# Performance work log

Measured on AMD Instinct MI355X. Metric: run time of the kernel, lower is better.

The kernel has to match this reference:

```python
import jax, jax.numpy as jnp
import numpy as np

INV_TEMP = 100.0


def setup_inputs() -> dict:
    key = jax.random.key(0)
    k1, k2, k3 = jax.random.split(key, 3)
    B, C, J, Hh, Wh = 64, 4, 17, 96, 96
    heatmaps = jax.random.normal(k1, (B * C, J, Hh, Wh), dtype=jnp.float32)
    projection_matrices = jax.random.normal(k2, (B, C, 3, 4), dtype=jnp.float32)
    confidences = jax.random.uniform(k3, (B, C, J), dtype=jnp.float32)
    return {
        "heatmaps": heatmaps,
        "projection_matrices": projection_matrices,
        "confidences": confidences,
        "H_img": 384,
        "W_img": 384,
    }


def _softargmax(heatmaps):
    # heatmaps: (B*C, J, Hh, Wh) -> keypoints (B*C, J, 2) as (x, y)
    bc, J, Hh, Wh = heatmaps.shape
    hm = jax.nn.softmax((heatmaps * INV_TEMP).reshape(bc, J, Hh * Wh), axis=-1)
    hm = hm.reshape(bc, J, Hh, Wh)
    xs = jnp.arange(Wh, dtype=hm.dtype)
    ys = jnp.arange(Hh, dtype=hm.dtype)
    kx = jnp.einsum('bjhw,w->bj', hm, xs)  # x = width index (grid c=0)
    ky = jnp.einsum('bjhw,h->bj', hm, ys)  # y = height index (grid c=1)
    return jnp.stack([kx, ky], axis=-1)


def _dlt(P, kp2d, conf):
    # P: (B,C,3,4), kp2d: (B,C,J,2), conf: (B,C,J) -> (B,J,3)
    B, C, J = kp2d.shape[:3]
    # A[b,c,j,i,:] = P[b,c,2,:]*kp2d[b,c,j,i] - P[b,c,i,:], scaled by conf
    A = (P[:, :, None, 2:3, :] * kp2d[:, :, :, :, None]
         - P[:, :, None, :2, :]) * conf[:, :, :, None, None]  # (B,C,J,2,4)
    A = A.transpose(0, 2, 1, 3, 4).reshape(B, J, 2 * C, 4)
    _, _, Vh = jnp.linalg.svd(A, full_matrices=False)  # Vh: (B,J,4,4)
    homo = Vh[..., 3, :]  # smallest right singular vector, (B,J,4)
    return homo[..., :3] / homo[..., 3:4]


def reference(heatmaps, projection_matrices, confidences, H_img, W_img):
    B, C = projection_matrices.shape[:2]
    bc, J, Hh, Wh = heatmaps.shape
    kp = _softargmax(heatmaps)  # (B*C, J, 2)
    # faithful (quirky) rescale: x *= H/Hh, y *= W/Wh as in original code
    scale = jnp.array([H_img / Hh, W_img / Wh], dtype=kp.dtype)
    kp = (kp * scale).reshape(B, C, J, 2)
    return _dlt(projection_matrices, kp, confidences)
```

## Files before the change

kernel.cpp:

```cpp
#include <hip/hip_runtime.h>

#define B_NUM 64
#define C_NUM 4
#define J_NUM 17
#define HH 96
#define WW 96
#define HWSZ (HH * WW)

__device__ __forceinline__ float waveMax(float v) {
#pragma unroll
  for (int o = 32; o > 0; o >>= 1) v = fmaxf(v, __shfl_xor(v, o));
  return v;
}
__device__ __forceinline__ float waveSum(float v) {
#pragma unroll
  for (int o = 32; o > 0; o >>= 1) v += __shfl_xor(v, o);
  return v;
}

__global__ __launch_bounds__(256) void softargmax_k(
    const float* __restrict__ hm, const int* __restrict__ Hp,
    const int* __restrict__ Wp, float* __restrict__ kp) {
  const int r = blockIdx.x;
  const int t = threadIdx.x;
  const float4* row = (const float4*)(hm + (size_t)r * HWSZ);

  float m = -3.4e38f;
  float se = 0.f, sx = 0.f, sy = 0.f;
#pragma unroll
  for (int k = 0; k < 9; ++k) {
    const float4 v = row[k * 256 + t];
    const int base = k * 1024 + t * 4;
    const int h = base / WW;
    const int w0 = base - h * WW;
    const float c = fmaxf(fmaxf(v.x, v.y), fmaxf(v.z, v.w));
    const float mn = fmaxf(m, c);
    const float f = __expf(100.f * (m - mn));
    m = mn;
    se *= f; sx *= f; sy *= f;
    const float a = -100.f * mn;
    const float e0 = __expf(fmaf(100.f, v.x, a));
    const float e1 = __expf(fmaf(100.f, v.y, a));
    const float e2 = __expf(fmaf(100.f, v.z, a));
    const float e3 = __expf(fmaf(100.f, v.w, a));
    const float esum = (e0 + e1) + (e2 + e3);
    se += esum;
    sy = fmaf(esum, (float)h, sy);
    sx += fmaf(esum, (float)w0, fmaf(2.f, e2, fmaf(3.f, e3, e1)));
  }

  const float M = waveMax(m);
  const float fw = __expf(100.f * (m - M));
  se = waveSum(se * fw);
  sx = waveSum(sx * fw);
  sy = waveSum(sy * fw);

  __shared__ float s[4][4];
  const int wid = t >> 6, lane = t & 63;
  if (lane == 0) { s[wid][0] = M; s[wid][1] = se; s[wid][2] = sx; s[wid][3] = sy; }
  __syncthreads();
  if (t == 0) {
    const float MM = fmaxf(fmaxf(s[0][0], s[1][0]), fmaxf(s[2][0], s[3][0]));
    float SE = 0.f, SX = 0.f, SY = 0.f;
#pragma unroll
    for (int i = 0; i < 4; ++i) {
      const float f = __expf(100.f * (s[i][0] - MM));
      SE = fmaf(s[i][1], f, SE);
      SX = fmaf(s[i][2], f, SX);
      SY = fmaf(s[i][3], f, SY);
    }
    const float scx = (float)Hp[0] / (float)HH;
    const float scy = (float)Wp[0] / (float)WW;
    ((float2*)kp)[r] = make_float2(SX / SE * scx, SY / SE * scy);
  }
}

__global__ __launch_bounds__(256) void dlt_k(
    const float* __restrict__ P, const float* __restrict__ conf,
    const float* __restrict__ kp, float* __restrict__ out) {
  const int idx = blockIdx.x * blockDim.x + threadIdx.x;
  if (idx >= B_NUM * J_NUM) return;
  const int b = idx / J_NUM;
  const int j = idx - b * J_NUM;

  double M[4][4];
#pragma unroll
  for (int a = 0; a < 4; ++a)
#pragma unroll
    for (int bb = 0; bb < 4; ++bb) M[a][bb] = 0.0;

#pragma unroll
  for (int c = 0; c < C_NUM; ++c) {
    const float* Pm = P + ((size_t)(b * C_NUM + c)) * 12;
    const float cf = conf[(b * C_NUM + c) * J_NUM + j];
    const float2 xy = ((const float2*)kp)[(b * C_NUM + c) * J_NUM + j];
    double row0[4], row1[4];
#pragma unroll
    for (int l = 0; l < 4; ++l) {
      const double p2 = (double)Pm[8 + l];
      row0[l] = (p2 * (double)xy.x - (double)Pm[l]) * (double)cf;
      row1[l] = (p2 * (double)xy.y - (double)Pm[4 + l]) * (double)cf;
    }
#pragma unroll
    for (int a = 0; a < 4; ++a)
#pragma unroll
      for (int bb = 0; bb < 4; ++bb)
        M[a][bb] += row0[a] * row0[bb] + row1[a] * row1[bb];
  }

  double V[4][4];
#pragma unroll
  for (int a = 0; a < 4; ++a)
#pragma unroll
    for (int bb = 0; bb < 4; ++bb) V[a][bb] = (a == bb) ? 1.0 : 0.0;

  for (int sweep = 0; sweep < 8; ++sweep) {
#pragma unroll
    for (int p = 0; p < 3; ++p) {
#pragma unroll
      for (int q = p + 1; q < 4; ++q) {
        const double d = M[p][q];
        if (fabs(d) < 1e-300) continue;
        const double a = M[p][p], bq = M[q][q];
        const double theta = (bq - a) / (2.0 * d);
        const double tt = (theta >= 0.0 ? 1.0 : -1.0) /
                          (fabs(theta) + sqrt(theta * theta + 1.0));
        const double cc = 1.0 / sqrt(tt * tt + 1.0);
        const double ss = tt * cc;
#pragma unroll
        for (int k = 0; k < 4; ++k) {
          if (k == p || k == q) continue;
          const double mkp = M[k][p], mkq = M[k][q];
          M[k][p] = M[p][k] = cc * mkp - ss * mkq;
          M[k][q] = M[q][k] = ss * mkp + cc * mkq;
        }
        M[p][p] = a - tt * d;
        M[q][q] = bq + tt * d;
        M[p][q] = M[q][p] = 0.0;
#pragma unroll
        for (int k = 0; k < 4; ++k) {
          const double vkp = V[k][p], vkq = V[k][q];
          V[k][p] = cc * vkp - ss * vkq;
          V[k][q] = ss * vkp + cc * vkq;
        }
      }
    }
  }

  int mi = 0;
  double mv = M[0][0];
#pragma unroll
  for (int i = 1; i < 4; ++i)
    if (M[i][i] < mv) { mv = M[i][i]; mi = i; }
  const double h3 = V[3][mi];
  out[idx * 3 + 0] = (float)(V[0][mi] / h3);
  out[idx * 3 + 1] = (float)(V[1][mi] / h3);
  out[idx * 3 + 2] = (float)(V[2][mi] / h3);
}

extern "C" void kernel_launch(void* const* d_in, const int* in_sizes, int n_in,
                              void* d_out, int out_size, void* d_ws, size_t ws_size,
                              hipStream_t stream) {
  const float* hm = (const float*)d_in[0];
  const float* P = (const float*)d_in[1];
  const float* conf = (const float*)d_in[2];
  const int* Hp = (const int*)d_in[3];
  const int* Wp = (const int*)d_in[4];
  float* out = (float*)d_out;
  float* kp = (float*)d_ws;

  softargmax_k<<<B_NUM * C_NUM * J_NUM, 256, 0, stream>>>(hm, Hp, Wp, kp);
  dlt_k<<<(B_NUM * J_NUM + 255) / 256, 256, 0, stream>>>(P, conf, kp, out);
}
```

Measured before the change: 242.0 us.

## Map one wavefront per softmax row with double-buffered register prefetch

Each heatmap row is now handled by a single 64-lane wavefront instead of a 256-thread block, so the shared-memory cross-wave reduction and __syncthreads are gone. Each lane loads 9 float4 values per batch and prefetches the next batch into registers, which raises memory-level parallelism per wave. The online max is updated once per batch rather than once per float4. exp is computed as exp2f with a pre-scaled constant. The costs are higher register pressure from 72 live floats per lane, which may lower occupancy, and more serial work per wave.

```diff
diff --git a/kernel.cpp b/kernel.cpp
--- a/kernel.cpp
+++ b/kernel.cpp
@@ -6,6 +6,8 @@
 #define HH 96
 #define WW 96
 #define HWSZ (HH * WW)
+#define NROWS (B_NUM * C_NUM * J_NUM)
+#define K100 144.26950408889634f
 
 __device__ __forceinline__ float waveMax(float v) {
 #pragma unroll
@@ -21,57 +23,57 @@
 __global__ __launch_bounds__(256) void softargmax_k(
     const float* __restrict__ hm, const int* __restrict__ Hp,
     const int* __restrict__ Wp, float* __restrict__ kp) {
-  const int r = blockIdx.x;
-  const int t = threadIdx.x;
-  const float4* row = (const float4*)(hm + (size_t)r * HWSZ);
+  const int gw = (blockIdx.x * blockDim.x + threadIdx.x) >> 6;
+  const int lane = threadIdx.x & 63;
+  const float4* row = (const float4*)(hm + (size_t)gw * HWSZ);
 
-  float m = -3.4e38f;
-  float se = 0.f, sx = 0.f, sy = 0.f;
+  float m = -3.4e38f, se = 0.f, sx = 0.f, sy = 0.f;
+  float4 cur[9], nxt[9];
 #pragma unroll
-  for (int k = 0; k < 9; ++k) {
-    const float4 v = row[k * 256 + t];
-    const int base = k * 1024 + t * 4;
-    const int h = base / WW;
-    const int w0 = base - h * WW;
-    const float c = fmaxf(fmaxf(v.x, v.y), fmaxf(v.z, v.w));
+  for (int i = 0; i < 9; ++i) cur[i] = row[i * 64 + lane];
+
+#pragma unroll
+  for (int b = 0; b < 4; ++b) {
+    if (b < 3) {
+#pragma unroll
+      for (int i = 0; i < 9; ++i) nxt[i] = row[(b + 1) * 576 + i * 64 + lane];
+    }
+    float c = -3.4e38f;
+#pragma unroll
+    for (int i = 0; i < 9; ++i)
+      c = fmaxf(c, fmaxf(fmaxf(cur[i].x, cur[i].y), fmaxf(cur[i].z, cur[i].w)));
     const float mn = fmaxf(m, c);
-    const float f = __expf(100.f * (m - mn));
+    const float f = exp2f(K100 * (m - mn));
     m = mn;
     se *= f; sx *= f; sy *= f;
-    const float a = -100.f * mn;
-    const float e0 = __expf(fmaf(100.f, v.x, a));
-    const float e1 = __expf(fmaf(100.f, v.y, a));
-    const float e2 = __expf(fmaf(100.f, v.z, a));
-    const float e3 = __expf(fmaf(100.f, v.w, a));
-    const float esum = (e0 + e1) + (e2 + e3);
-    se += esum;
-    sy = fmaf(esum, (float)h, sy);
-    sx += fmaf(esum, (float)w0, fmaf(2.f, e2, fmaf(3.f, e3, e1)));
+    const float a = -K100 * mn;
+#pragma unroll
+    for (int i = 0; i < 9; ++i) {
+      const int flat = (b * 9 + i) * 256 + lane * 4;
+      const int h = flat / WW;
+      const int w0 = flat - h * WW;
+      const float e0 = exp2f(fmaf(K100, cur[i].x, a));
+      const float e1 = exp2f(fmaf(K100, cur[i].y, a));
+      const float e2 = exp2f(fmaf(K100, cur[i].z, a));
+      const float e3 = exp2f(fmaf(K100, cur[i].w, a));
+      const float esum = (e0 + e1) + (e2 + e3);
+      se += esum;
+      sy = fmaf(esum, (float)h, sy);
+      sx += fmaf(esum, (float)w0, fmaf(2.f, e2, fmaf(3.f, e3, e1)));
+    }
+#pragma unroll
+    for (int i = 0; i < 9; ++i) cur[i] = nxt[i];
   }
 
   const float M = waveMax(m);
-  const float fw = __expf(100.f * (m - M));
+  const float fw = exp2f(K100 * (m - M));
   se = waveSum(se * fw);
   sx = waveSum(sx * fw);
   sy = waveSum(sy * fw);
-
-  __shared__ float s[4][4];
-  const int wid = t >> 6, lane = t & 63;
-  if (lane == 0) { s[wid][0] = M; s[wid][1] = se; s[wid][2] = sx; s[wid][3] = sy; }
-  __syncthreads();
-  if (t == 0) {
-    const float MM = fmaxf(fmaxf(s[0][0], s[1][0]), fmaxf(s[2][0], s[3][0]));
-    float SE = 0.f, SX = 0.f, SY = 0.f;
-#pragma unroll
-    for (int i = 0; i < 4; ++i) {
-      const float f = __expf(100.f * (s[i][0] - MM));
-      SE = fmaf(s[i][1], f, SE);
-      SX = fmaf(s[i][2], f, SX);
-      SY = fmaf(s[i][3], f, SY);
-    }
+  if (lane == 0) {
     const float scx = (float)Hp[0] / (float)HH;
     const float scy = (float)Wp[0] / (float)WW;
-    ((float2*)kp)[r] = make_float2(SX / SE * scx, SY / SE * scy);
+    ((float2*)kp)[gw] = make_float2(sx / se * scx, sy / se * scy);
   }
 }
 
@@ -169,6 +171,6 @@
   float* out = (float*)d_out;
   float* kp = (float*)d_ws;
 
-  softargmax_k<<<B_NUM * C_NUM * J_NUM, 256, 0, stream>>>(hm, Hp, Wp, kp);
+  softargmax_k<<<NROWS / 4, 256, 0, stream>>>(hm, Hp, Wp, kp);
   dlt_k<<<(B_NUM * J_NUM + 255) / 256, 256, 0, stream>>>(P, conf, kp, out);
 }
```

Result: no change. 245.3 us (+1.4%).
